# Performance work log

Hardware: AMD Instinct MI355X
Metric: run time of the kernel (lower is better)

The kernel has to match this reference:

```python
import math
import jax, jax.numpy as jnp
import numpy as np

EMBED_LEN = 512  # self.dk in the torch module (used for scaling, NOT the head dim)


def setup_inputs() -> dict:
    key = jax.random.key(0)
    kq, kk, kv = jax.random.split(key, 3)
    B, H, S, D = 2, 8, 4096, 64
    queries = jax.random.normal(kq, (B, H, S, D), dtype=jnp.float32)
    keys = jax.random.normal(kk, (B, H, S, D), dtype=jnp.float32)
    # NOTE: values enters as [B, S, H, D]; forward transposes dims (1,2).
    values = jax.random.normal(kv, (B, S, H, D), dtype=jnp.float32)
    return {"queries": queries, "keys": keys, "values": values}


def reference(queries, keys, values):
    # compatibility = Q @ K^T / sqrt(dk), dk = embed_len (512), mask=None branch
    scores = jnp.einsum("bhqd,bhkd->bhqk", queries, keys) / math.sqrt(EMBED_LEN)
    attn = jax.nn.softmax(scores, axis=3)
    # torch.transpose(values, 1, 2): [B,S,H,D] -> [B,H,S,D]
    v = jnp.swapaxes(values, 1, 2)
    return jnp.einsum("bhqk,bhkd->bhqd", attn, v)
```

## Files before the change

kernel.cpp:

```cpp
#include <hip/hip_runtime.h>

typedef __attribute__((ext_vector_type(8))) short bf16x8;
typedef __attribute__((ext_vector_type(4))) short s16x4;
typedef __attribute__((ext_vector_type(4))) float f32x4;

#define MFMA16 __builtin_amdgcn_mfma_f32_16x16x32_bf16

#if __has_builtin(__builtin_amdgcn_exp2f)
__device__ __forceinline__ float exp2_raw(float x) { return __builtin_amdgcn_exp2f(x); }
#else
__device__ __forceinline__ float exp2_raw(float x) {
    float r;
    asm volatile("v_exp_f32 %0, %1" : "=v"(r) : "v"(x));
    return r;
}
#endif

__device__ __forceinline__ short bf16s(float f) {
    __bf16 h = (__bf16)f;
    return __builtin_bit_cast(short, h);
}

__device__ __forceinline__ void gload16(const char* g, char* l) {
    __builtin_amdgcn_global_load_lds(
        (const __attribute__((address_space(1))) unsigned int*)g,
        (__attribute__((address_space(3))) unsigned int*)l, 16, 0, 0);
}

__global__ __launch_bounds__(256) void prep_kv(const float* __restrict__ K,
                                               const float* __restrict__ V,
                                               char* __restrict__ Kimg,
                                               char* __restrict__ Vimg) {
    const int t = threadIdx.x;
    if (blockIdx.x < 1024) {
        const int bid = blockIdx.x;
        const int c = t & 3, r = t >> 2;
        char* dst = Kimg + (size_t)bid * 8192;
        const float* src = K + (size_t)bid * 4096 + (size_t)r * 64 + c * 16;
        float e[16];
        *(float4*)(e)      = *(const float4*)(src);
        *(float4*)(e + 4)  = *(const float4*)(src + 4);
        *(float4*)(e + 8)  = *(const float4*)(src + 8);
        *(float4*)(e + 12) = *(const float4*)(src + 12);
#pragma unroll
        for (int lg = 0; lg < 4; ++lg) {
            s16x4 wv;
#pragma unroll
            for (int j = 0; j < 4; ++j) wv[j] = bf16s(e[lg * 4 + j]);
            const unsigned f = (unsigned)((((c >> 1) * 4 + lg) ^ (r & 7)));
            *(s16x4*)(dst + r * 128 + f * 16 + (c & 1) * 8) = wv;
        }
    } else {
        const int bid = blockIdx.x - 1024;
        const int head = bid >> 6, it = bid & 63;
        const int b = head >> 3, h = head & 7;
        const int d = t & 63, f0 = t >> 6;
        char* dst = Vimg + (size_t)bid * 8192;
#pragma unroll
        for (int ff = 0; ff < 2; ++ff) {
            const int f = f0 + ff * 4;
            const int hh = f >> 2, lg = f & 3;
            const int kv0 = hh * 32 + lg * 4;
            const float* src = V + ((size_t)b * 4096 + it * 64 + kv0) * 512 + h * 64 + d;
            bf16x8 wv;
#pragma unroll
            for (int j = 0; j < 4; ++j) wv[j]     = bf16s(src[(size_t)j * 512]);
#pragma unroll
            for (int j = 0; j < 4; ++j) wv[4 + j] = bf16s(src[(size_t)(16 + j) * 512]);
            *(bf16x8*)(dst + d * 128 + (unsigned)((f ^ (d & 7)) * 16)) = wv;
        }
    }
}

__global__ __launch_bounds__(64, 2)
void sdpa_fa_kernel(const float* __restrict__ Q, const char* __restrict__ Kimg,
                    const char* __restrict__ Vimg, float* __restrict__ P0,
                    unsigned short* __restrict__ Pb, float* __restrict__ LS) {
    __shared__ __align__(16) char LDS[8192];

    const int bid  = blockIdx.x;
    const int xcd  = bid & 7;
    const int idx  = bid >> 3;
    const int head = xcd + 8 * (idx >> 8);
    const int rem  = idx & 255;
    const int kvh  = rem >> 6;
    const int qt   = rem & 63;
    const int hb   = head * 64 + kvh * 16;

    const int l   = threadIdx.x;
    const int lg  = l >> 4;
    const int lc  = l & 15;
    const int lc7 = lc & 7;

    const float C1 = (float)(1.4426950408889634 / 22.627416997969522);

    bf16x8 qf[4][2];
#pragma unroll
    for (int qi = 0; qi < 4; ++qi) {
        const int qrow = qt * 64 + qi * 16 + lc;
        const float* qp = Q + ((size_t)head * 4096 + qrow) * 64;
#pragma unroll
        for (int half = 0; half < 2; ++half) {
            bf16x8 f;
#pragma unroll
            for (int j = 0; j < 4; ++j) {
                f[j]     = bf16s(qp[half * 32 + lg * 4 + j] * C1);
                f[4 + j] = bf16s(qp[half * 32 + 16 + lg * 4 + j] * C1);
            }
            qf[qi][half] = f;
        }
    }

    bf16x8 ones;
#pragma unroll
    for (int j = 0; j < 8; ++j) ones[j] = (short)0x3F80;

    f32x4 Oa[4][4];
    f32x4 ls[4];
#pragma unroll
    for (int qi = 0; qi < 4; ++qi) {
        ls[qi] = (f32x4){0.f, 0.f, 0.f, 0.f};
#pragma unroll
        for (int dt = 0; dt < 4; ++dt) Oa[qi][dt] = (f32x4){0.f, 0.f, 0.f, 0.f};
    }

    unsigned off0[4], off1[4];
#pragma unroll
    for (int g = 0; g < 4; ++g) {
        off0[g] = (unsigned)((g * 16 + lc) * 128 + (((0 + lg) ^ lc7) * 16));
        off1[g] = (unsigned)((g * 16 + lc) * 128 + (((4 + lg) ^ lc7) * 16));
    }

    auto stage_k = [&](int it) {
        const char* gk = Kimg + (size_t)(hb + it) * 8192 + l * 16;
#pragma unroll
        for (int i = 0; i < 8; ++i) gload16(gk + i * 1024, LDS + i * 1024);
    };
    auto stage_v = [&](int it) {
        const char* gv = Vimg + (size_t)(hb + it) * 8192 + l * 16;
#pragma unroll
        for (int i = 0; i < 8; ++i) gload16(gv + i * 1024, LDS + i * 1024);
    };

    stage_k(0);

#pragma unroll 1
    for (int it = 0; it < 16; ++it) {
        const int nx = (it + 1) & 15;

        asm volatile("s_waitcnt vmcnt(0)" ::: "memory");
        __builtin_amdgcn_sched_barrier(0);
        bf16x8 kf[4][2];
#pragma unroll
        for (int g = 0; g < 4; ++g) {
            kf[g][0] = *(const bf16x8*)(LDS + off0[g]);
            kf[g][1] = *(const bf16x8*)(LDS + off1[g]);
        }
        asm volatile("s_waitcnt lgkmcnt(0)" ::: "memory");
        __builtin_amdgcn_sched_barrier(0);
        stage_v(it);
        __builtin_amdgcn_sched_barrier(0);

        f32x4 st0[4][2], st1[4][2];
        __builtin_amdgcn_s_setprio(1);
#pragma unroll
        for (int g2 = 0; g2 < 2; ++g2)
#pragma unroll
            for (int qi = 0; qi < 4; ++qi) {
                f32x4 a = (f32x4){0.f, 0.f, 0.f, 0.f};
                a = MFMA16(kf[g2][0], qf[qi][0], a, 0, 0, 0);
                a = MFMA16(kf[g2][1], qf[qi][1], a, 0, 0, 0);
                st0[qi][g2] = a;
            }
#pragma unroll
        for (int g2 = 0; g2 < 2; ++g2)
#pragma unroll
            for (int qi = 0; qi < 4; ++qi) {
                f32x4 a = (f32x4){0.f, 0.f, 0.f, 0.f};
                a = MFMA16(kf[g2 + 2][0], qf[qi][0], a, 0, 0, 0);
                a = MFMA16(kf[g2 + 2][1], qf[qi][1], a, 0, 0, 0);
                st1[qi][g2] = a;
#pragma unroll
                for (int r = 0; r < 4; ++r) st0[qi][g2][r] = exp2_raw(st0[qi][g2][r]);
            }
        __builtin_amdgcn_s_setprio(0);

        bf16x8 pfr0[4];
#pragma unroll
        for (int qi = 0; qi < 4; ++qi) {
            bf16x8 f;
#pragma unroll
            for (int j = 0; j < 4; ++j) {
                f[j]     = bf16s(st0[qi][0][j]);
                f[4 + j] = bf16s(st0[qi][1][j]);
            }
            pfr0[qi] = f;
        }

        asm volatile("s_waitcnt vmcnt(0)" ::: "memory");
        __builtin_amdgcn_sched_barrier(0);
        bf16x8 vf[4][2];
#pragma unroll
        for (int dt = 0; dt < 4; ++dt) {
            vf[dt][0] = *(const bf16x8*)(LDS + off0[dt]);
            vf[dt][1] = *(const bf16x8*)(LDS + off1[dt]);
        }
        asm volatile("s_waitcnt lgkmcnt(0)" ::: "memory");
        __builtin_amdgcn_sched_barrier(0);
        stage_k(nx);
        __builtin_amdgcn_sched_barrier(0);

        __builtin_amdgcn_s_setprio(1);
#pragma unroll
        for (int qi = 0; qi < 4; ++qi) {
            ls[qi] = MFMA16(pfr0[qi], ones, ls[qi], 0, 0, 0);
#pragma unroll
            for (int r = 0; r < 4; ++r) st1[qi][0][r] = exp2_raw(st1[qi][0][r]);
            Oa[qi][0] = MFMA16(pfr0[qi], vf[0][0], Oa[qi][0], 0, 0, 0);
            Oa[qi][1] = MFMA16(pfr0[qi], vf[1][0], Oa[qi][1], 0, 0, 0);
#pragma unroll
            for (int r = 0; r < 4; ++r) st1[qi][1][r] = exp2_raw(st1[qi][1][r]);
            Oa[qi][2] = MFMA16(pfr0[qi], vf[2][0], Oa[qi][2], 0, 0, 0);
            Oa[qi][3] = MFMA16(pfr0[qi], vf[3][0], Oa[qi][3], 0, 0, 0);
        }
        __builtin_amdgcn_s_setprio(0);

        bf16x8 pfr1[4];
#pragma unroll
        for (int qi = 0; qi < 4; ++qi) {
            bf16x8 f;
#pragma unroll
            for (int j = 0; j < 4; ++j) {
                f[j]     = bf16s(st1[qi][0][j]);
                f[4 + j] = bf16s(st1[qi][1][j]);
            }
            pfr1[qi] = f;
        }

        __builtin_amdgcn_s_setprio(1);
#pragma unroll
        for (int qi = 0; qi < 4; ++qi) {
            ls[qi] = MFMA16(pfr1[qi], ones, ls[qi], 0, 0, 0);
#pragma unroll
            for (int dt = 0; dt < 4; ++dt)
                Oa[qi][dt] = MFMA16(pfr1[qi], vf[dt][1], Oa[qi][dt], 0, 0, 0);
        }
        __builtin_amdgcn_s_setprio(0);
    }

    float* lsw = LS + kvh * 65536;
    if (kvh == 0) {
#pragma unroll
        for (int qi = 0; qi < 4; ++qi)
#pragma unroll
            for (int r = 0; r < 4; ++r) {
                const int q = qt * 64 + qi * 16 + lg * 4 + r;
                float* og = P0 + ((size_t)head * 4096 + q) * 64 + lc;
#pragma unroll
                for (int dt = 0; dt < 4; ++dt) og[dt * 16] = Oa[qi][dt][r];
                if (lc == 0) lsw[head * 4096 + q] = ls[qi][r];
            }
    } else {
        unsigned short* Pq = Pb + (size_t)(kvh - 1) * 4194304;
#pragma unroll
        for (int qi = 0; qi < 4; ++qi)
#pragma unroll
            for (int r = 0; r < 4; ++r) {
                const int q = qt * 64 + qi * 16 + lg * 4 + r;
                unsigned short* og = Pq + ((size_t)head * 4096 + q) * 64 + lc;
#pragma unroll
                for (int dt = 0; dt < 4; ++dt)
                    og[dt * 16] = (unsigned short)bf16s(Oa[qi][dt][r]);
                if (lc == 0) lsw[head * 4096 + q] = ls[qi][r];
            }
    }
}

__global__ __launch_bounds__(256) void merge_out(const unsigned short* __restrict__ Pb,
                                                 const float* __restrict__ LS,
                                                 float* __restrict__ Out) {
    const int i = (blockIdx.x * 256 + threadIdx.x) * 4;
    const int hq = i >> 6;
    const float inv = 1.0f / (LS[hq] + LS[65536 + hq] + LS[131072 + hq] + LS[196608 + hq]);
    const float4 a = *(const float4*)(Out + i);
    float s[4] = {a.x, a.y, a.z, a.w};
#pragma unroll
    for (int p = 0; p < 3; ++p) {
        ushort4 u = *(const ushort4*)(Pb + (size_t)p * 4194304 + i);
        s[0] += __builtin_bit_cast(float, (unsigned)u.x << 16);
        s[1] += __builtin_bit_cast(float, (unsigned)u.y << 16);
        s[2] += __builtin_bit_cast(float, (unsigned)u.z << 16);
        s[3] += __builtin_bit_cast(float, (unsigned)u.w << 16);
    }
    float4 r;
    r.x = s[0] * inv; r.y = s[1] * inv; r.z = s[2] * inv; r.w = s[3] * inv;
    *(float4*)(Out + i) = r;
}

extern "C" void kernel_launch(void* const* d_in, const int* in_sizes, int n_in,
                              void* d_out, int out_size, void* d_ws, size_t ws_size,
                              hipStream_t stream) {
    const float* Q = (const float*)d_in[0];
    const float* K = (const float*)d_in[1];
    const float* V = (const float*)d_in[2];
    float* Out = (float*)d_out;
    char* Kimg = (char*)d_ws;
    char* Vimg = (char*)d_ws + (size_t)8388608;
    unsigned short* Pb = (unsigned short*)((char*)d_ws + 16777216);
    float* LS = (float*)((char*)d_ws + (size_t)41943040);
    prep_kv<<<dim3(2048), dim3(256), 0, stream>>>(K, V, Kimg, Vimg);
    sdpa_fa_kernel<<<dim3(4096), dim3(64), 0, stream>>>(Q, Kimg, Vimg, Out, Pb, LS);
    merge_out<<<dim3(4096), dim3(256), 0, stream>>>(Pb, LS, Out);
}
```

Baseline: 95.58 us.

## Merge KV-split partials in LDS within one block, dropping merge kernel

The four KV-split partial attention outputs for a query tile now come from four waves in one 256-thread block, not from four separate single-wave blocks. Waves 1-3 write bf16 partial outputs and row sums to their own LDS region, and wave 0 reduces them and writes the normalized output. This removes the separate merge kernel launch and the global round trip of partials and sums. The cost is larger LDS per block (about 33KB), a block-wide barrier at the end, and different occupancy (3 blocks of 4 waves per CU).

```diff
diff --git a/kernel.cpp b/kernel.cpp
--- a/kernel.cpp
+++ b/kernel.cpp
@@ -72,26 +72,28 @@
     }
 }
 
-__global__ __launch_bounds__(64, 2)
+__global__ __launch_bounds__(256, 3)
 void sdpa_fa_kernel(const float* __restrict__ Q, const char* __restrict__ Kimg,
-                    const char* __restrict__ Vimg, float* __restrict__ P0,
-                    unsigned short* __restrict__ Pb, float* __restrict__ LS) {
-    __shared__ __align__(16) char LDS[8192];
+                    const char* __restrict__ Vimg, float* __restrict__ Out) {
+    __shared__ __align__(16) char LDS[33792];
 
     const int bid  = blockIdx.x;
     const int xcd  = bid & 7;
     const int idx  = bid >> 3;
-    const int head = xcd + 8 * (idx >> 8);
-    const int rem  = idx & 255;
-    const int kvh  = rem >> 6;
-    const int qt   = rem & 63;
-    const int hb   = head * 64 + kvh * 16;
-
-    const int l   = threadIdx.x;
+    const int head = xcd + 8 * (idx >> 6);
+    const int qt   = idx & 63;
+
+    const int t   = threadIdx.x;
+    const int w   = t >> 6;
+    const int l   = t & 63;
     const int lg  = l >> 4;
     const int lc  = l & 15;
     const int lc7 = lc & 7;
 
+    const int hb = head * 64 + w * 16;
+    char* LB = LDS + w * 8448;
+    float* LSw = (float*)(LB + 8192);
+
     const float C1 = (float)(1.4426950408889634 / 22.627416997969522);
 
     bf16x8 qf[4][2];
@@ -134,27 +136,25 @@
     auto stage_k = [&](int it) {
         const char* gk = Kimg + (size_t)(hb + it) * 8192 + l * 16;
 #pragma unroll
-        for (int i = 0; i < 8; ++i) gload16(gk + i * 1024, LDS + i * 1024);
+        for (int i = 0; i < 8; ++i) gload16(gk + i * 1024, LB + i * 1024);
     };
     auto stage_v = [&](int it) {
         const char* gv = Vimg + (size_t)(hb + it) * 8192 + l * 16;
 #pragma unroll
-        for (int i = 0; i < 8; ++i) gload16(gv + i * 1024, LDS + i * 1024);
+        for (int i = 0; i < 8; ++i) gload16(gv + i * 1024, LB + i * 1024);
     };
 
     stage_k(0);
 
 #pragma unroll 1
     for (int it = 0; it < 16; ++it) {
-        const int nx = (it + 1) & 15;
-
         asm volatile("s_waitcnt vmcnt(0)" ::: "memory");
         __builtin_amdgcn_sched_barrier(0);
         bf16x8 kf[4][2];
 #pragma unroll
         for (int g = 0; g < 4; ++g) {
-            kf[g][0] = *(const bf16x8*)(LDS + off0[g]);
-            kf[g][1] = *(const bf16x8*)(LDS + off1[g]);
+            kf[g][0] = *(const bf16x8*)(LB + off0[g]);
+            kf[g][1] = *(const bf16x8*)(LB + off1[g]);
         }
         asm volatile("s_waitcnt lgkmcnt(0)" ::: "memory");
         __builtin_amdgcn_sched_barrier(0);
@@ -202,12 +202,12 @@
         bf16x8 vf[4][2];
 #pragma unroll
         for (int dt = 0; dt < 4; ++dt) {
-            vf[dt][0] = *(const bf16x8*)(LDS + off0[dt]);
-            vf[dt][1] = *(const bf16x8*)(LDS + off1[dt]);
+            vf[dt][0] = *(const bf16x8*)(LB + off0[dt]);
+            vf[dt][1] = *(const bf16x8*)(LB + off1[dt]);
         }
         asm volatile("s_waitcnt lgkmcnt(0)" ::: "memory");
         __builtin_amdgcn_sched_barrier(0);
-        stage_k(nx);
+        if (it + 1 < 16) stage_k(it + 1);
         __builtin_amdgcn_sched_barrier(0);
 
         __builtin_amdgcn_s_setprio(1);
@@ -248,53 +248,45 @@
         __builtin_amdgcn_s_setprio(0);
     }
 
-    float* lsw = LS + kvh * 65536;
-    if (kvh == 0) {
+    if (w != 0) {
+        unsigned short* Ob = (unsigned short*)LB;
 #pragma unroll
         for (int qi = 0; qi < 4; ++qi)
 #pragma unroll
             for (int r = 0; r < 4; ++r) {
-                const int q = qt * 64 + qi * 16 + lg * 4 + r;
-                float* og = P0 + ((size_t)head * 4096 + q) * 64 + lc;
-#pragma unroll
-                for (int dt = 0; dt < 4; ++dt) og[dt * 16] = Oa[qi][dt][r];
-                if (lc == 0) lsw[head * 4096 + q] = ls[qi][r];
-            }
-    } else {
-        unsigned short* Pq = Pb + (size_t)(kvh - 1) * 4194304;
+                const int q = qi * 16 + lg * 4 + r;
+#pragma unroll
+                for (int dt = 0; dt < 4; ++dt)
+                    Ob[q * 64 + dt * 16 + lc] = (unsigned short)bf16s(Oa[qi][dt][r]);
+                if (lc == 0) LSw[q] = ls[qi][r];
+            }
+    }
+    __syncthreads();
+    if (w == 0) {
 #pragma unroll
         for (int qi = 0; qi < 4; ++qi)
 #pragma unroll
             for (int r = 0; r < 4; ++r) {
-                const int q = qt * 64 + qi * 16 + lg * 4 + r;
-                unsigned short* og = Pq + ((size_t)head * 4096 + q) * 64 + lc;
-#pragma unroll
-                for (int dt = 0; dt < 4; ++dt)
-                    og[dt * 16] = (unsigned short)bf16s(Oa[qi][dt][r]);
-                if (lc == 0) lsw[head * 4096 + q] = ls[qi][r];
-            }
-    }
-}
-
-__global__ __launch_bounds__(256) void merge_out(const unsigned short* __restrict__ Pb,
-                                                 const float* __restrict__ LS,
-                                                 float* __restrict__ Out) {
-    const int i = (blockIdx.x * 256 + threadIdx.x) * 4;
-    const int hq = i >> 6;
-    const float inv = 1.0f / (LS[hq] + LS[65536 + hq] + LS[131072 + hq] + LS[196608 + hq]);
-    const float4 a = *(const float4*)(Out + i);
-    float s[4] = {a.x, a.y, a.z, a.w};
-#pragma unroll
-    for (int p = 0; p < 3; ++p) {
-        ushort4 u = *(const ushort4*)(Pb + (size_t)p * 4194304 + i);
-        s[0] += __builtin_bit_cast(float, (unsigned)u.x << 16);
-        s[1] += __builtin_bit_cast(float, (unsigned)u.y << 16);
-        s[2] += __builtin_bit_cast(float, (unsigned)u.z << 16);
-        s[3] += __builtin_bit_cast(float, (unsigned)u.w << 16);
-    }
-    float4 r;
-    r.x = s[0] * inv; r.y = s[1] * inv; r.z = s[2] * inv; r.w = s[3] * inv;
-    *(float4*)(Out + i) = r;
+                const int q = qi * 16 + lg * 4 + r;
+                float tot = ls[qi][r];
+#pragma unroll
+                for (int wv = 1; wv < 4; ++wv)
+                    tot += *(const float*)(LDS + wv * 8448 + 8192 + q * 4);
+                const float inv = 1.0f / tot;
+                float* og = Out + ((size_t)head * 4096 + qt * 64 + q) * 64 + lc;
+#pragma unroll
+                for (int dt = 0; dt < 4; ++dt) {
+                    float s = Oa[qi][dt][r];
+#pragma unroll
+                    for (int wv = 1; wv < 4; ++wv) {
+                        const unsigned short u = *(const unsigned short*)
+                            (LDS + wv * 8448 + (q * 64 + dt * 16 + lc) * 2);
+                        s += __builtin_bit_cast(float, (unsigned)u << 16);
+                    }
+                    og[dt * 16] = s * inv;
+                }
+            }
+    }
 }
 
 extern "C" void kernel_launch(void* const* d_in, const int* in_sizes, int n_in,
@@ -306,9 +298,6 @@
     float* Out = (float*)d_out;
     char* Kimg = (char*)d_ws;
     char* Vimg = (char*)d_ws + (size_t)8388608;
-    unsigned short* Pb = (unsigned short*)((char*)d_ws + 16777216);
-    float* LS = (float*)((char*)d_ws + (size_t)41943040);
     prep_kv<<<dim3(2048), dim3(256), 0, stream>>>(K, V, Kimg, Vimg);
-    sdpa_fa_kernel<<<dim3(4096), dim3(64), 0, stream>>>(Q, Kimg, Vimg, Out, Pb, LS);
-    merge_out<<<dim3(4096), dim3(256), 0, stream>>>(Pb, LS, Out);
-}
+    sdpa_fa_kernel<<<dim3(1024), dim3(256), 0, stream>>>(Q, Kimg, Vimg, Out);
+}
```

Result: slower. 262.2 us (+174.3%).
